# Optimization experiments

Measured on AMD Instinct MI355X. Metric: run time of the kernel, lower is better.

## Reference

```python
import jax, jax.numpy as jnp
import numpy as np

EMBED_DIM = 1024
NUM_HEADS = 16
HEAD_DIM = EMBED_DIM // NUM_HEADS
B, QL, CL = 2, 2048, 2048


def setup_inputs() -> dict:
    key = jax.random.key(0)
    ks = jax.random.split(key, 10)
    s = 1.0 / np.sqrt(EMBED_DIM)  # torch Linear default init scale (approx)
    inp = {
        "query": jax.random.normal(ks[0], (B, QL, EMBED_DIM), jnp.float32),
        "context": jax.random.normal(ks[1], (B, CL, EMBED_DIM), jnp.float32),
        "Wq": jax.random.normal(ks[2], (EMBED_DIM, EMBED_DIM), jnp.float32) * s,
        "bq": jnp.zeros((EMBED_DIM,), jnp.float32),
        "Wk": jax.random.normal(ks[3], (EMBED_DIM, EMBED_DIM), jnp.float32) * s,
        "bk": jnp.zeros((EMBED_DIM,), jnp.float32),
        "Wv": jax.random.normal(ks[4], (EMBED_DIM, EMBED_DIM), jnp.float32) * s,
        "bv": jnp.zeros((EMBED_DIM,), jnp.float32),
        "Wo": jax.random.normal(ks[5], (EMBED_DIM, EMBED_DIM), jnp.float32) * s,
        "bo": jnp.zeros((EMBED_DIM,), jnp.float32),
    }
    return inp


def reference(query, context, Wq, bq, Wk, bk, Wv, bv, Wo, bo):
    b, ql, _ = query.shape
    cl = context.shape[1]
    # projections (torch Linear: x @ W.T + b; here W stored as (in, out) so x @ W + b)
    Q = (query @ Wq + bq).reshape(b, ql, NUM_HEADS, HEAD_DIM).transpose(0, 2, 1, 3)
    K = (context @ Wk + bk).reshape(b, cl, NUM_HEADS, HEAD_DIM).transpose(0, 2, 1, 3)
    V = (context @ Wv + bv).reshape(b, cl, NUM_HEADS, HEAD_DIM).transpose(0, 2, 1, 3)
    # scores [b, h, ql, cl]
    scores = jnp.einsum("bhqd,bhkd->bhqk", Q, K) / np.sqrt(HEAD_DIM).astype(np.float32)
    probs = jax.nn.softmax(scores, axis=-1)
    # dropout=0.0 (eval): identity
    attended = jnp.einsum("bhqk,bhkd->bhqd", probs, V)
    attended = attended.transpose(0, 2, 1, 3).reshape(b, ql, EMBED_DIM)
    return attended @ Wo + bo
```

## Files before the change

### kernel.cpp

```cpp
#include <hip/hip_runtime.h>
#include <hip/hip_bf16.h>
#include <stdint.h>

#define EMBED 1024
#define NH 16
#define HD 64
#define BATCH 2
#define QLEN 2048
#define CLEN 2048

typedef short short8 __attribute__((ext_vector_type(8)));
typedef unsigned short ushort8v __attribute__((ext_vector_type(8)));
typedef float f32x4 __attribute__((ext_vector_type(4)));
typedef float f32x16 __attribute__((ext_vector_type(16)));
typedef uint32_t u32x4 __attribute__((ext_vector_type(4)));

#define QSCALE 0.18033688f

__device__ __forceinline__ void async_load16(const void* g, void* l) {
    __builtin_amdgcn_global_load_lds((const __attribute__((address_space(1))) void*)g,
                                     (__attribute__((address_space(3))) void*)l, 16, 0, 0);
}

__device__ __forceinline__ uint32_t pack2(float a, float b) {
    float2 f{a, b};
    __hip_bfloat162 t = __float22bfloat162_rn(f);
    uint32_t u;
    __builtin_memcpy(&u, &t, 4);
    return u;
}

__global__ void prep(const float* __restrict__ query, const float* __restrict__ context,
                     __hip_bfloat16* __restrict__ qbf, __hip_bfloat16* __restrict__ cbf,
                     const float* __restrict__ W0, const float* __restrict__ W1,
                     const float* __restrict__ W2, const float* __restrict__ W3,
                     __hip_bfloat16* __restrict__ T0, __hip_bfloat16* __restrict__ T1,
                     __hip_bfloat16* __restrict__ T2, __hip_bfloat16* __restrict__ T3) {
    const int y = blockIdx.y;
    const int tid = threadIdx.x;
    if (y < 2) {
        const float* src = y ? context : query;
        __hip_bfloat16* dst = y ? cbf : qbf;
#pragma unroll
        for (int k = 0; k < 4; k++) {
            const int i = (blockIdx.x * 1024 + k * 256 + tid) * 4;
            float4 v = *(const float4*)(src + i);
            __hip_bfloat16 h[4];
            h[0] = __float2bfloat16(v.x);
            h[1] = __float2bfloat16(v.y);
            h[2] = __float2bfloat16(v.z);
            h[3] = __float2bfloat16(v.w);
            *(ushort4*)(dst + i) = *(const ushort4*)h;
        }
    } else {
        const int z = y - 2;
        const float* W = z == 0 ? W0 : z == 1 ? W1 : z == 2 ? W2 : W3;
        __hip_bfloat16* Wt = z == 0 ? T0 : z == 1 ? T1 : z == 2 ? T2 : T3;
        __shared__ float t[32][33];
        const int tx = tid & 31, ty = tid >> 5;
        const int n0 = (blockIdx.x & 31) * 32, k0 = (blockIdx.x >> 5) * 32;
#pragma unroll
        for (int r = 0; r < 4; r++)
            t[ty * 4 + r][tx] = W[(size_t)(k0 + ty * 4 + r) * EMBED + n0 + tx];
        __syncthreads();
#pragma unroll
        for (int r = 0; r < 4; r++)
            Wt[(size_t)(n0 + ty * 4 + r) * EMBED + k0 + tx] = __float2bfloat16(t[tx][ty * 4 + r]);
    }
}

__device__ __forceinline__ void gemm128_acc(
    const __hip_bfloat16* __restrict__ A, const __hip_bfloat16* __restrict__ Bt,
    int m0, int n0, __hip_bfloat16* As, __hip_bfloat16* Bs, f32x4 acc[4][4]) {
    const int K = EMBED;
    const int tid = threadIdx.x;
    const int wave = __builtin_amdgcn_readfirstlane(tid >> 6);
    const int lane = tid & 63, l15 = lane & 15, quad = lane >> 4;
    const int wm = (wave >> 1) * 64, wn = (wave & 1) * 64;
    const int srow = tid >> 2, sseg = (tid & 3) * 8;
    for (int k0 = 0; k0 < K; k0 += 32) {
        __syncthreads();
#pragma unroll
        for (int s = 0; s < 2; s++) {
            async_load16(A + (size_t)(m0 + s * 64 + srow) * K + k0 + sseg,
                         As + (size_t)(s * 256 + wave * 64) * 8);
            async_load16(Bt + (size_t)(n0 + s * 64 + srow) * K + k0 + sseg,
                         Bs + (size_t)(s * 256 + wave * 64) * 8);
        }
        __syncthreads();
        short8 af[4], bf[4];
#pragma unroll
        for (int t = 0; t < 4; t++) {
            af[t] = *(const short8*)(As + (wm + t * 16 + l15) * 32 + quad * 8);
            bf[t] = *(const short8*)(Bs + (wn + t * 16 + l15) * 32 + quad * 8);
        }
#pragma unroll
        for (int mt = 0; mt < 4; mt++)
#pragma unroll
            for (int nt = 0; nt < 4; nt++)
                acc[mt][nt] = __builtin_amdgcn_mfma_f32_16x16x32_bf16(af[mt], bf[nt], acc[mt][nt], 0, 0, 0);
    }
}

__global__ __launch_bounds__(256, 3) void proj128(
    const __hip_bfloat16* __restrict__ qbf, const __hip_bfloat16* __restrict__ cbf,
    const __hip_bfloat16* __restrict__ Wqt, const __hip_bfloat16* __restrict__ Wkvt,
    const float* __restrict__ bq, const float* __restrict__ bk, const float* __restrict__ bv,
    __hip_bfloat16* __restrict__ Qp, __hip_bfloat16* __restrict__ Kp, __hip_bfloat16* __restrict__ Vtr) {
    __shared__ __hip_bfloat16 smem[8704];
    __hip_bfloat16* As = smem;
    __hip_bfloat16* Bs = smem + 4096;
    const int j = blockIdx.x;
    const int blk = (j & 7) * 96 + (j >> 3);
    const __hip_bfloat16 *A, *Bt;
    int m0, n0;
    if (blk < 256) {
        A = qbf; Bt = Wqt; m0 = (blk >> 3) * 128; n0 = (blk & 7) * 128;
    } else {
        const int f = blk - 256;
        A = cbf; Bt = Wkvt; m0 = (f >> 4) * 128; n0 = (f & 15) * 128;
    }
    f32x4 acc[4][4] = {};
    gemm128_acc(A, Bt, m0, n0, As, Bs, acc);

    const int tid = threadIdx.x;
    const int wave = __builtin_amdgcn_readfirstlane(tid >> 6);
    const int lane = tid & 63, l15 = lane & 15, quad = lane >> 4;
    const int wm = (wave >> 1) * 64, wn = (wave & 1) * 64;

    if (blk >= 256 && n0 >= 1024) {
        const int cb = n0 - 1024;
        const int b2 = m0 >> 11;
        const int tokb = m0 & 2047;
        __hip_bfloat16* T = smem;
#pragma unroll
        for (int hh = 0; hh < 2; hh++) {
            __syncthreads();
            if ((wn >> 6) == hh) {
#pragma unroll
                for (int nt = 0; nt < 4; nt++) {
                    const int cn = nt * 16 + l15;
                    const float bvv = bv[cb + hh * 64 + cn];
#pragma unroll
                    for (int mt = 0; mt < 4; mt++) {
                        const int m = wm + mt * 16 + quad * 4;
                        __hip_bfloat16 vb[4];
#pragma unroll
                        for (int r = 0; r < 4; r++) vb[r] = __float2bfloat16(acc[mt][nt][r] + bvv);
                        *(ushort4*)(T + cn * 136 + m) = *(const ushort4*)vb;
                    }
                }
            }
            __syncthreads();
            const int r = tid >> 2;
            const int seg = (tid & 3) * 32;
            unsigned short* dst = (unsigned short*)Vtr +
                (size_t)(b2 * 1024 + cb + hh * 64 + r) * CLEN + tokb + seg;
            const unsigned short* srcp = (const unsigned short*)(T + r * 136 + seg);
#pragma unroll
            for (int u = 0; u < 4; u++)
                *(ushort8v*)(dst + u * 8) = *(const ushort8v*)(srcp + u * 8);
        }
    } else {
        const bool isQ = (blk < 256);
        const float* bias = isQ ? bq : bk;
        __hip_bfloat16* C = isQ ? Qp : Kp;
        const float sc = isQ ? QSCALE : 1.0f;
#pragma unroll
        for (int mt = 0; mt < 4; mt++) {
#pragma unroll
            for (int nt = 0; nt < 4; nt++) {
                const int c = n0 + wn + nt * 16 + l15;
                const float bvv = bias[c];
                const int r0 = m0 + wm + mt * 16 + quad * 4;
#pragma unroll
                for (int r = 0; r < 4; r++)
                    C[(size_t)(r0 + r) * 1024 + c] = __float2bfloat16((acc[mt][nt][r] + bvv) * sc);
            }
        }
    }
}

__global__ __launch_bounds__(256, 4) void oproj(
    const __hip_bfloat16* __restrict__ A, const __hip_bfloat16* __restrict__ Bt,
    const float* __restrict__ bias, float* __restrict__ C) {
    __shared__ __hip_bfloat16 As[64 * 32];
    __shared__ __hip_bfloat16 Bs[128 * 32];
    const int K = EMBED, N = EMBED;
    const int j = blockIdx.x;
    const int L = (j & 7) * 64 + (j >> 3);
    const int m0 = (L >> 3) * 64, n0 = (L & 7) * 128;
    const int tid = threadIdx.x;
    const int wave = __builtin_amdgcn_readfirstlane(tid >> 6);
    const int lane = tid & 63, l15 = lane & 15, quad = lane >> 4;
    const int wm = (wave & 1) * 32, wn = (wave >> 1) * 64;
    const int srow = tid >> 2, sseg = (tid & 3) * 8;
    f32x4 acc[2][4] = {};
    for (int k0 = 0; k0 < K; k0 += 32) {
        __syncthreads();
        async_load16(A + (size_t)(m0 + srow) * K + k0 + sseg, As + (size_t)(wave * 64) * 8);
#pragma unroll
        for (int s = 0; s < 2; s++)
            async_load16(Bt + (size_t)(n0 + s * 64 + srow) * K + k0 + sseg,
                         Bs + (size_t)(s * 256 + wave * 64) * 8);
        __syncthreads();
        short8 af[2], bf[4];
#pragma unroll
        for (int t = 0; t < 2; t++)
            af[t] = *(const short8*)(As + (wm + t * 16 + l15) * 32 + quad * 8);
#pragma unroll
        for (int t = 0; t < 4; t++)
            bf[t] = *(const short8*)(Bs + (wn + t * 16 + l15) * 32 + quad * 8);
#pragma unroll
        for (int mt = 0; mt < 2; mt++)
#pragma unroll
            for (int nt = 0; nt < 4; nt++)
                acc[mt][nt] = __builtin_amdgcn_mfma_f32_16x16x32_bf16(af[mt], bf[nt], acc[mt][nt], 0, 0, 0);
    }
#pragma unroll
    for (int mt = 0; mt < 2; mt++) {
#pragma unroll
        for (int nt = 0; nt < 4; nt++) {
            const int c = n0 + wn + nt * 16 + l15;
            const float bvv = bias[c];
            const int r0 = m0 + wm + mt * 16 + quad * 4;
#pragma unroll
            for (int r = 0; r < 4; r++)
                C[(size_t)(r0 + r) * N + c] = acc[mt][nt][r] + bvv;
        }
    }
}

__global__ __launch_bounds__(256, 2) void flash_attn(
    const __hip_bfloat16* __restrict__ Q, const __hip_bfloat16* __restrict__ K,
    const __hip_bfloat16* __restrict__ Vt, __hip_bfloat16* __restrict__ O) {
    __shared__ __hip_bfloat16 Ks[2][64 * 64];
    __shared__ __hip_bfloat16 Vs[2][64 * 64];
    const int tid = threadIdx.x;
    const int wave = __builtin_amdgcn_readfirstlane(tid >> 6);
    const int lane = tid & 63, l31 = lane & 31, hbit = lane >> 5;
    const int j = blockIdx.x;
    const int L = (j & 7) * 64 + (j >> 3);
    const int hy = L >> 4;
    const int b = hy >> 4, h = hy & 15;
    const int q0 = (L & 15) * 128;
    const size_t kbase = (size_t)b * CLEN * EMBED + (size_t)h * HD;
    const size_t vtbase = (size_t)((b * NH + h) * HD) * CLEN;
    const int srow8 = lane >> 3;
    const int sgb = (lane & 7) ^ srow8;

    const __hip_bfloat16* qptr =
        Q + (size_t)(b * QLEN + q0 + wave * 32 + l31) * EMBED + h * HD + hbit * 8;
    short8 qf[4];
#pragma unroll
    for (int t = 0; t < 4; t++) qf[t] = *(const short8*)(qptr + t * 16);

    f32x16 o[2] = {};
    float lsA = 0.f, lsB = 0.f;

#pragma unroll
    for (int u = 0; u < 2; u++) {
        const int i = wave * 2 + u;
        async_load16(K + kbase + (size_t)(i * 8 + srow8) * EMBED + (sgb ^ i) * 8,
                     Ks[0] + i * 512);
        async_load16(Vt + vtbase + (size_t)(i * 8 + srow8) * CLEN + (sgb ^ i) * 8,
                     Vs[0] + i * 512);
    }

    for (int t = 0; t < 32; ++t) {
        const int cur = t & 1;
        __syncthreads();
        if (t < 31) {
            const int cn = (t + 1) * 64;
#pragma unroll
            for (int u = 0; u < 2; u++) {
                const int i = wave * 2 + u;
                async_load16(K + kbase + (size_t)(cn + i * 8 + srow8) * EMBED + (sgb ^ i) * 8,
                             Ks[cur ^ 1] + i * 512);
                async_load16(Vt + vtbase + (size_t)(i * 8 + srow8) * CLEN + cn + (sgb ^ i) * 8,
                             Vs[cur ^ 1] + i * 512);
            }
        }
        const __hip_bfloat16* stK = Ks[cur];
        const __hip_bfloat16* stV = Vs[cur];

#pragma unroll
        for (int mc = 0; mc < 2; mc++) {
            const int row = mc * 32 + l31;
            const int rsw = (row & 7) ^ (row >> 3);
            const __hip_bfloat16* kr = stK + row * 64;
            f32x16 sv = {};
            __builtin_amdgcn_s_setprio(1);
#pragma unroll
            for (int kc = 0; kc < 4; kc++) {
                short8 kf = *(const short8*)(kr + ((2 * kc + hbit) ^ rsw) * 8);
                sv = __builtin_amdgcn_mfma_f32_32x32x16_bf16(kf, qf[kc], sv, 0, 0, 0);
            }
            __builtin_amdgcn_s_setprio(0);
            uint32_t dw[8];
#pragma unroll
            for (int i = 0; i < 8; i++) {
                const float p0 = __builtin_amdgcn_exp2f(sv[2 * i]);
                const float p1 = __builtin_amdgcn_exp2f(sv[2 * i + 1]);
                if (i & 1) lsB += p0 + p1; else lsA += p0 + p1;
                dw[i] = pack2(p0, p1);
            }
#pragma unroll
            for (int tp = 0; tp < 2; tp++) {
                u32x4 fb;
#if __has_builtin(__builtin_amdgcn_permlane32_swap)
                {
                    auto s02 = __builtin_amdgcn_permlane32_swap(dw[4 * tp + 0], dw[4 * tp + 2], false, false);
                    auto s13 = __builtin_amdgcn_permlane32_swap(dw[4 * tp + 1], dw[4 * tp + 3], false, false);
                    fb[0] = s02[0];
                    fb[1] = s13[0];
                    fb[2] = s02[1];
                    fb[3] = s13[1];
                }
#else
                {
                    const uint32_t a0 = hbit ? dw[4 * tp + 2] : dw[4 * tp + 0];
                    const uint32_t a1 = hbit ? dw[4 * tp + 3] : dw[4 * tp + 1];
                    const uint32_t b0 = hbit ? dw[4 * tp + 0] : dw[4 * tp + 2];
                    const uint32_t b1 = hbit ? dw[4 * tp + 1] : dw[4 * tp + 3];
                    const uint32_t x0 = (uint32_t)__shfl_xor((int)b0, 32);
                    const uint32_t x1 = (uint32_t)__shfl_xor((int)b1, 32);
                    fb[0] = hbit ? x0 : a0;
                    fb[1] = hbit ? x1 : a1;
                    fb[2] = hbit ? a0 : x0;
                    fb[3] = hbit ? a1 : x1;
                }
#endif
                const short8 pfr = __builtin_bit_cast(short8, fb);
                const int kc2 = mc * 2 + tp;
                __builtin_amdgcn_s_setprio(1);
#pragma unroll
                for (int dm = 0; dm < 2; dm++) {
                    const int vrow = dm * 32 + l31;
                    const int vsw = (vrow & 7) ^ (vrow >> 3);
                    short8 vf = *(const short8*)(stV + vrow * 64 + ((2 * kc2 + hbit) ^ vsw) * 8);
                    o[dm] = __builtin_amdgcn_mfma_f32_32x32x16_bf16(vf, pfr, o[dm], 0, 0, 0);
                }
                __builtin_amdgcn_s_setprio(0);
            }
        }
    }

    float lsum = lsA + lsB;
    lsum += __shfl_xor(lsum, 32);
    const float inv = 1.0f / lsum;
    const int q = q0 + wave * 32 + l31;
    __hip_bfloat16* orow = O + (size_t)(b * QLEN + q) * EMBED + h * HD;
#pragma unroll
    for (int dm = 0; dm < 2; dm++) {
#pragma unroll
        for (int g = 0; g < 4; g++) {
            __hip_bfloat16 ob[4];
#pragma unroll
            for (int r = 0; r < 4; r++) ob[r] = __float2bfloat16(o[dm][g * 4 + r] * inv);
            *(ushort4*)(orow + dm * 32 + hbit * 4 + g * 8) = *(const ushort4*)ob;
        }
    }
}

extern "C" void kernel_launch(void* const* d_in, const int* in_sizes, int n_in,
                              void* d_out, int out_size, void* d_ws, size_t ws_size,
                              hipStream_t stream) {
    const float* query = (const float*)d_in[0];
    const float* context = (const float*)d_in[1];
    const float* Wq = (const float*)d_in[2];
    const float* bq = (const float*)d_in[3];
    const float* Wk = (const float*)d_in[4];
    const float* bk = (const float*)d_in[5];
    const float* Wv = (const float*)d_in[6];
    const float* bv = (const float*)d_in[7];
    const float* Wo = (const float*)d_in[8];
    const float* bo = (const float*)d_in[9];
    float* out = (float*)d_out;

    const int NTOK = BATCH * QLEN;
    const int NACT = NTOK * EMBED;
    const int NW = EMBED * EMBED;

    __hip_bfloat16* qbf = (__hip_bfloat16*)d_ws;
    __hip_bfloat16* cbf = qbf + NACT;
    __hip_bfloat16* Wqt = cbf + NACT;
    __hip_bfloat16* Wkt = Wqt + NW;
    __hip_bfloat16* Wvt = Wkt + NW;
    __hip_bfloat16* Wot = Wvt + NW;
    __hip_bfloat16* Qp = Wot + NW;
    __hip_bfloat16* Kp = Qp + NACT;
    __hip_bfloat16* Vtr = Kp + NACT;
    __hip_bfloat16* att = Vtr + NACT;

    prep<<<dim3(1024, 6), 256, 0, stream>>>(query, context, qbf, cbf,
                                            Wq, Wk, Wv, Wo, Wqt, Wkt, Wvt, Wot);

    proj128<<<768, 256, 0, stream>>>(qbf, cbf, Wqt, Wkt, bq, bk, bv, Qp, Kp, Vtr);

    flash_attn<<<512, 256, 0, stream>>>(Qp, Kp, Vtr, att);

    oproj<<<512, 256, 0, stream>>>(att, Wot, bo, out);
}
```

Measured before the change: 205.1 us.

## Restructure flash attention inner loop to batch LDS loads and interleave two score MFMAs

Loads all K and V fragments for the tile from LDS up front, computes both 32-row score blocks with interleaved independent MFMA chains, then does the exp/pack and PV MFMAs. Global load addresses become incrementally advanced pointers instead of being recomputed each iteration. The goal is more instruction-level parallelism and better hiding of LDS latency. The cost is higher VGPR pressure, which could hurt occupancy under launch_bounds(256,2).

```diff
diff --git a/kernel.cpp b/kernel.cpp
--- a/kernel.cpp
+++ b/kernel.cpp
@@ -248,6 +248,7 @@
     const size_t vtbase = (size_t)((b * NH + h) * HD) * CLEN;
     const int srow8 = lane >> 3;
     const int sgb = (lane & 7) ^ srow8;
+    const int i0 = wave * 2, i1 = wave * 2 + 1;
 
     const __hip_bfloat16* qptr =
         Q + (size_t)(b * QLEN + q0 + wave * 32 + l31) * EMBED + h * HD + hbit * 8;
@@ -256,62 +257,85 @@
     for (int t = 0; t < 4; t++) qf[t] = *(const short8*)(qptr + t * 16);
 
     f32x16 o[2] = {};
-    float lsA = 0.f, lsB = 0.f;
-
-#pragma unroll
-    for (int u = 0; u < 2; u++) {
-        const int i = wave * 2 + u;
-        async_load16(K + kbase + (size_t)(i * 8 + srow8) * EMBED + (sgb ^ i) * 8,
-                     Ks[0] + i * 512);
-        async_load16(Vt + vtbase + (size_t)(i * 8 + srow8) * CLEN + (sgb ^ i) * 8,
-                     Vs[0] + i * 512);
-    }
+    float lsA = 0.f, lsB = 0.f, lsC = 0.f, lsD = 0.f;
+
+    const __hip_bfloat16* pk0 = K + kbase + (size_t)(i0 * 8 + srow8) * EMBED + (sgb ^ i0) * 8;
+    const __hip_bfloat16* pk1 = K + kbase + (size_t)(i1 * 8 + srow8) * EMBED + (sgb ^ i1) * 8;
+    const __hip_bfloat16* pv0 = Vt + vtbase + (size_t)(i0 * 8 + srow8) * CLEN + (sgb ^ i0) * 8;
+    const __hip_bfloat16* pv1 = Vt + vtbase + (size_t)(i1 * 8 + srow8) * CLEN + (sgb ^ i1) * 8;
+
+    async_load16(pk0, Ks[0] + i0 * 512);
+    async_load16(pk1, Ks[0] + i1 * 512);
+    async_load16(pv0, Vs[0] + i0 * 512);
+    async_load16(pv1, Vs[0] + i1 * 512);
+    pk0 += (size_t)64 * EMBED; pk1 += (size_t)64 * EMBED;
+    pv0 += 64; pv1 += 64;
+
+    const int rsw0 = (l31 & 7) ^ (l31 >> 3);
+    const int rsw1 = (l31 & 7) ^ ((32 + l31) >> 3);
 
     for (int t = 0; t < 32; ++t) {
         const int cur = t & 1;
         __syncthreads();
         if (t < 31) {
-            const int cn = (t + 1) * 64;
-#pragma unroll
-            for (int u = 0; u < 2; u++) {
-                const int i = wave * 2 + u;
-                async_load16(K + kbase + (size_t)(cn + i * 8 + srow8) * EMBED + (sgb ^ i) * 8,
-                             Ks[cur ^ 1] + i * 512);
-                async_load16(Vt + vtbase + (size_t)(i * 8 + srow8) * CLEN + cn + (sgb ^ i) * 8,
-                             Vs[cur ^ 1] + i * 512);
-            }
+            async_load16(pk0, Ks[cur ^ 1] + i0 * 512);
+            async_load16(pk1, Ks[cur ^ 1] + i1 * 512);
+            async_load16(pv0, Vs[cur ^ 1] + i0 * 512);
+            async_load16(pv1, Vs[cur ^ 1] + i1 * 512);
+            pk0 += (size_t)64 * EMBED; pk1 += (size_t)64 * EMBED;
+            pv0 += 64; pv1 += 64;
         }
         const __hip_bfloat16* stK = Ks[cur];
         const __hip_bfloat16* stV = Vs[cur];
 
+        short8 kf[2][4];
+#pragma unroll
+        for (int kc = 0; kc < 4; kc++) {
+            kf[0][kc] = *(const short8*)(stK + l31 * 64 + ((2 * kc + hbit) ^ rsw0) * 8);
+            kf[1][kc] = *(const short8*)(stK + (32 + l31) * 64 + ((2 * kc + hbit) ^ rsw1) * 8);
+        }
+        f32x16 sv0 = {}, sv1 = {};
+        __builtin_amdgcn_s_setprio(1);
+#pragma unroll
+        for (int kc = 0; kc < 4; kc++) {
+            sv0 = __builtin_amdgcn_mfma_f32_32x32x16_bf16(kf[0][kc], qf[kc], sv0, 0, 0, 0);
+            sv1 = __builtin_amdgcn_mfma_f32_32x32x16_bf16(kf[1][kc], qf[kc], sv1, 0, 0, 0);
+        }
+        __builtin_amdgcn_s_setprio(0);
+
+        short8 vf[2][4];
+#pragma unroll
+        for (int dm = 0; dm < 2; dm++) {
+            const int vrow = dm * 32 + l31;
+            const int vsw = (vrow & 7) ^ (vrow >> 3);
+            const __hip_bfloat16* vr = stV + vrow * 64;
+#pragma unroll
+            for (int k2 = 0; k2 < 4; k2++)
+                vf[dm][k2] = *(const short8*)(vr + ((2 * k2 + hbit) ^ vsw) * 8);
+        }
+
+        uint32_t dw[2][8];
+#pragma unroll
+        for (int i = 0; i < 8; i++) {
+            const float a0 = __builtin_amdgcn_exp2f(sv0[2 * i]);
+            const float a1 = __builtin_amdgcn_exp2f(sv0[2 * i + 1]);
+            const float b0 = __builtin_amdgcn_exp2f(sv1[2 * i]);
+            const float b1 = __builtin_amdgcn_exp2f(sv1[2 * i + 1]);
+            if (i & 1) { lsB += a0 + a1; lsD += b0 + b1; }
+            else       { lsA += a0 + a1; lsC += b0 + b1; }
+            dw[0][i] = pack2(a0, a1);
+            dw[1][i] = pack2(b0, b1);
+        }
+
 #pragma unroll
         for (int mc = 0; mc < 2; mc++) {
-            const int row = mc * 32 + l31;
-            const int rsw = (row & 7) ^ (row >> 3);
-            const __hip_bfloat16* kr = stK + row * 64;
-            f32x16 sv = {};
-            __builtin_amdgcn_s_setprio(1);
-#pragma unroll
-            for (int kc = 0; kc < 4; kc++) {
-                short8 kf = *(const short8*)(kr + ((2 * kc + hbit) ^ rsw) * 8);
-                sv = __builtin_amdgcn_mfma_f32_32x32x16_bf16(kf, qf[kc], sv, 0, 0, 0);
-            }
-            __builtin_amdgcn_s_setprio(0);
-            uint32_t dw[8];
-#pragma unroll
-            for (int i = 0; i < 8; i++) {
-                const float p0 = __builtin_amdgcn_exp2f(sv[2 * i]);
-                const float p1 = __builtin_amdgcn_exp2f(sv[2 * i + 1]);
-                if (i & 1) lsB += p0 + p1; else lsA += p0 + p1;
-                dw[i] = pack2(p0, p1);
-            }
 #pragma unroll
             for (int tp = 0; tp < 2; tp++) {
                 u32x4 fb;
 #if __has_builtin(__builtin_amdgcn_permlane32_swap)
                 {
-                    auto s02 = __builtin_amdgcn_permlane32_swap(dw[4 * tp + 0], dw[4 * tp + 2], false, false);
-                    auto s13 = __builtin_amdgcn_permlane32_swap(dw[4 * tp + 1], dw[4 * tp + 3], false, false);
+                    auto s02 = __builtin_amdgcn_permlane32_swap(dw[mc][4 * tp + 0], dw[mc][4 * tp + 2], false, false);
+                    auto s13 = __builtin_amdgcn_permlane32_swap(dw[mc][4 * tp + 1], dw[mc][4 * tp + 3], false, false);
                     fb[0] = s02[0];
                     fb[1] = s13[0];
                     fb[2] = s02[1];
@@ -319,10 +343,10 @@
                 }
 #else
                 {
-                    const uint32_t a0 = hbit ? dw[4 * tp + 2] : dw[4 * tp + 0];
-                    const uint32_t a1 = hbit ? dw[4 * tp + 3] : dw[4 * tp + 1];
-                    const uint32_t b0 = hbit ? dw[4 * tp + 0] : dw[4 * tp + 2];
-                    const uint32_t b1 = hbit ? dw[4 * tp + 1] : dw[4 * tp + 3];
+                    const uint32_t a0 = hbit ? dw[mc][4 * tp + 2] : dw[mc][4 * tp + 0];
+                    const uint32_t a1 = hbit ? dw[mc][4 * tp + 3] : dw[mc][4 * tp + 1];
+                    const uint32_t b0 = hbit ? dw[mc][4 * tp + 0] : dw[mc][4 * tp + 2];
+                    const uint32_t b1 = hbit ? dw[mc][4 * tp + 1] : dw[mc][4 * tp + 3];
                     const uint32_t x0 = (uint32_t)__shfl_xor((int)b0, 32);
                     const uint32_t x1 = (uint32_t)__shfl_xor((int)b1, 32);
                     fb[0] = hbit ? x0 : a0;
@@ -334,19 +358,14 @@
                 const short8 pfr = __builtin_bit_cast(short8, fb);
                 const int kc2 = mc * 2 + tp;
                 __builtin_amdgcn_s_setprio(1);
-#pragma unroll
-                for (int dm = 0; dm < 2; dm++) {
-                    const int vrow = dm * 32 + l31;
-                    const int vsw = (vrow & 7) ^ (vrow >> 3);
-                    short8 vf = *(const short8*)(stV + vrow * 64 + ((2 * kc2 + hbit) ^ vsw) * 8);
-                    o[dm] = __builtin_amdgcn_mfma_f32_32x32x16_bf16(vf, pfr, o[dm], 0, 0, 0);
-                }
+                o[0] = __builtin_amdgcn_mfma_f32_32x32x16_bf16(vf[0][kc2], pfr, o[0], 0, 0, 0);
+                o[1] = __builtin_amdgcn_mfma_f32_32x32x16_bf16(vf[1][kc2], pfr, o[1], 0, 0, 0);
                 __builtin_amdgcn_s_setprio(0);
             }
         }
     }
 
-    float lsum = lsA + lsB;
+    float lsum = (lsA + lsB) + (lsC + lsD);
     lsum += __shfl_xor(lsum, 32);
     const float inv = 1.0f / lsum;
     const int q = q0 + wave * 32 + l31;
```

Result: no change. 202.1 us (-1.4%).
